# Optimization experiments

Measured on AMD Instinct MI355X. Metric: run time of the kernel, lower is better.

## Reference

```python
import jax, jax.numpy as jnp
import numpy as np

EMBED_DIM = 1024
NUM_HEADS = 16
HEAD_DIM = EMBED_DIM // NUM_HEADS
THETA = 10000.0


def setup_inputs() -> dict:
    key = jax.random.key(0)
    ks = jax.random.split(key, 5)
    B, S, E = 2, 2048, EMBED_DIM
    x = jax.random.normal(ks[0], (B, S, E), dtype=jnp.float32)
    s = 1.0 / np.sqrt(E)
    Wq = jax.random.normal(ks[1], (E, E), dtype=jnp.float32) * s
    Wk = jax.random.normal(ks[2], (E, E), dtype=jnp.float32) * s
    Wv = jax.random.normal(ks[3], (E, E), dtype=jnp.float32) * s
    Wo = jax.random.normal(ks[4], (E, E), dtype=jnp.float32) * s
    bo = jnp.zeros((E,), dtype=jnp.float32)
    return {"x": x, "Wq": Wq, "Wk": Wk, "Wv": Wv, "Wo": Wo, "bo": bo}


def _apply_rope(t, cos, sin):
    # t: (B, H, S, D); cos, sin: (S, D/2)
    t1 = t[..., 0::2]
    t2 = t[..., 1::2]
    r1 = t1 * cos - t2 * sin
    r2 = t1 * sin + t2 * cos
    # interleave back: (..., D/2, 2) -> (..., D)
    return jnp.stack([r1, r2], axis=-1).reshape(t.shape)


def reference(x, Wq, Wk, Wv, Wo, bo):
    B, S, E = x.shape
    H, D = NUM_HEADS, HEAD_DIM
    scale = D ** -0.5

    # projections (torch Linear: y = x @ W.T)
    q = (x @ Wq.T).reshape(B, S, H, D).transpose(0, 2, 1, 3)
    k = (x @ Wk.T).reshape(B, S, H, D).transpose(0, 2, 1, 3)
    v = (x @ Wv.T).reshape(B, S, H, D).transpose(0, 2, 1, 3)

    # fixed RoPE freqs (temporal, non-learned)
    freqs = 1.0 / THETA ** (jnp.arange(0, D, 2, dtype=jnp.float32) / D)  # (D/2,)
    pos = jnp.arange(S, dtype=jnp.float32)
    angles = pos[:, None] * freqs[None, :]  # (S, D/2)
    cos, sin = jnp.cos(angles), jnp.sin(angles)

    q = _apply_rope(q, cos, sin)
    k = _apply_rope(k, cos, sin)

    attn = jnp.einsum('bhqd,bhkd->bhqk', q, k) * scale
    attn = jax.nn.softmax(attn, axis=-1)
    out = jnp.einsum('bhqk,bhkd->bhqd', attn, v)
    out = out.transpose(0, 2, 1, 3).reshape(B, S, E)
    return out @ Wo.T + bo
```

## Files before the change

kernel.cpp:

```cpp
#include <hip/hip_runtime.h>


typedef __attribute__((ext_vector_type(8))) short bf16x8;
typedef __attribute__((ext_vector_type(4))) float f32x4;
typedef unsigned short u16;
typedef unsigned int u32;

#define MFMA(a, b, c) __builtin_amdgcn_mfma_f32_16x16x32_bf16((a), (b), (c), 0, 0, 0)

#define GLOAD16(g, l)                                                        \
  __builtin_amdgcn_global_load_lds((const __attribute__((address_space(1))) void*)(g), \
                                   (__attribute__((address_space(3))) void*)(l), 16, 0, 0)

__device__ __forceinline__ float bf2f(u16 u) {
  union { u32 i; float f; } v; v.i = ((u32)u) << 16; return v.f;
}
__device__ __forceinline__ u16 f2bf(float f) {
  union { float f; u32 i; } v; v.f = f;
  u32 x = v.i;
  return (u16)((x + 0x7fffu + ((x >> 16) & 1u)) >> 16);
}

__global__ __launch_bounds__(256) void prep_kernel(
    const float* __restrict__ x, const float* __restrict__ Wq, const float* __restrict__ Wk,
    const float* __restrict__ Wv, const float* __restrict__ Wo, u16* __restrict__ xb,
    u16* __restrict__ Wqb, u16* __restrict__ Wkb, u16* __restrict__ Wvb, u16* __restrict__ Wob,
    float* __restrict__ cosT, float* __restrict__ sinT) {
  int bid = blockIdx.x;
  if (bid < 4096) {
    int i = bid * 256 + threadIdx.x;
    const float* src;
    u16* dst;
    int r;
    if (i < 524288) {
      src = x; dst = xb; r = i;
    } else {
      int k = i - 524288, sel = k >> 17;
      r = k & 131071;
      src = sel == 0 ? Wq : sel == 1 ? Wk : sel == 2 ? Wv : Wo;
      dst = sel == 0 ? Wqb : sel == 1 ? Wkb : sel == 2 ? Wvb : Wob;
    }
    const float4* p = (const float4*)src + 2 * (size_t)r;
    float4 a = p[0], b = p[1];
    bf16x8 o;
    o[0] = (short)f2bf(a.x); o[1] = (short)f2bf(a.y);
    o[2] = (short)f2bf(a.z); o[3] = (short)f2bf(a.w);
    o[4] = (short)f2bf(b.x); o[5] = (short)f2bf(b.y);
    o[6] = (short)f2bf(b.z); o[7] = (short)f2bf(b.w);
    *(bf16x8*)(dst + 8 * (size_t)r) = o;
  } else {
    int i = (bid - 4096) * 256 + threadIdx.x;
    int s = i >> 5, p = i & 31;
    float freq = powf(10000.0f, -(float)(2 * p) / 64.0f);
    float ang = (float)s * freq;
    cosT[i] = cosf(ang);
    sinT[i] = sinf(ang);
  }
}

template <int MODE>
__global__ __launch_bounds__(256) void gemm_bt_kernel(
    const u16* __restrict__ A, const u16* __restrict__ B0, const u16* __restrict__ B1,
    const u16* __restrict__ B2, u16* __restrict__ Qo, u16* __restrict__ Ko,
    u16* __restrict__ VT, const float* __restrict__ cosT, const float* __restrict__ sinT,
    float* __restrict__ Cf, const float* __restrict__ bias, int Ntot) {
  const int K = 1024;
  const int tid = threadIdx.x, lane = tid & 63, wid = tid >> 6;
  const int wr = wid >> 1, wc = wid & 1;
  const int m0 = blockIdx.y * 128;
  const int nt = blockIdx.x;
  const int n0 = nt * 128;
  const u16* Bt;
  int nloc0, sel;
  if (MODE == 0) {
    sel = nt >> 3;
    Bt = sel == 0 ? B0 : (sel == 1 ? B1 : B2);
    nloc0 = n0 & 1023;
  } else {
    sel = 0;
    Bt = B0;
    nloc0 = n0;
  }

  __shared__ u16 As[128 * 64];
  __shared__ u16 Bs[128 * 64];

  f32x4 acc[4][4];
#pragma unroll
  for (int i = 0; i < 4; i++)
#pragma unroll
    for (int j = 0; j < 4; j++) acc[i][j] = f32x4{0.f, 0.f, 0.f, 0.f};

  const int strow = tid >> 3;
  const int sgcol0 = (tid & 7) * 8;

  auto stage = [&](int k0) {
#pragma unroll
    for (int p = 0; p < 4; ++p) {
      int row = p * 32 + strow;
      int gcol = sgcol0 ^ ((row & 7) << 3);
      const u16* ga = A + (size_t)(m0 + row) * K + k0 + gcol;
      const u16* gb = Bt + (size_t)(nloc0 + row) * K + k0 + gcol;
      u16* la = As + (p * 256 + wid * 64) * 8;
      u16* lb = Bs + (p * 256 + wid * 64) * 8;
      GLOAD16(ga, la);
      GLOAD16(gb, lb);
    }
  };

  for (int k0 = 0; k0 < K; k0 += 64) {
    stage(k0);
    __syncthreads();
#pragma unroll
    for (int kk = 0; kk < 2; ++kk) {
      bf16x8 af[4], bfr[4];
#pragma unroll
      for (int i = 0; i < 4; ++i) {
        int row = wr * 64 + i * 16 + (lane & 15);
        int col = (kk * 32 + (lane >> 4) * 8) ^ ((row & 7) << 3);
        af[i] = *(const bf16x8*)(As + row * 64 + col);
      }
#pragma unroll
      for (int j = 0; j < 4; ++j) {
        int row = wc * 64 + j * 16 + (lane & 15);
        int col = (kk * 32 + (lane >> 4) * 8) ^ ((row & 7) << 3);
        bfr[j] = *(const bf16x8*)(Bs + row * 64 + col);
      }
#pragma unroll
      for (int i = 0; i < 4; ++i)
#pragma unroll
        for (int j = 0; j < 4; ++j) acc[i][j] = MFMA(af[i], bfr[j], acc[i][j]);
    }
    __syncthreads();
  }

  if (MODE == 1) {
#pragma unroll
    for (int i = 0; i < 4; ++i)
#pragma unroll
      for (int j = 0; j < 4; ++j)
#pragma unroll
        for (int r = 0; r < 4; ++r) {
          int row = m0 + wr * 64 + i * 16 + (lane >> 4) * 4 + r;
          int col = n0 + wc * 64 + j * 16 + (lane & 15);
          Cf[(size_t)row * Ntot + col] = acc[i][j][r] + bias[col];
        }
    return;
  }

  const int par = lane & 1;
  if (sel < 2) {
    u16* dst = sel == 0 ? Qo : Ko;
    const float mul = sel == 0 ? 0.125f : 1.0f;
#pragma unroll
    for (int i = 0; i < 4; ++i) {
      int rowb = m0 + wr * 64 + i * 16 + (lane >> 4) * 4;
      int s = rowb & 2047, b = rowb >> 11;
#pragma unroll
      for (int j = 0; j < 4; ++j) {
        int col = nloc0 + wc * 64 + j * 16 + (lane & 15);
        int h = col >> 6, dd = col & 63, p = dd >> 1;
        size_t base = ((size_t)(b * 16 + h) * 2048 + s) * 64 + (dd & ~1);
#pragma unroll
        for (int r = 0; r < 4; ++r) {
          float v = acc[i][j][r];
          float other = __shfl_xor(v, 1, 64);
          float t1 = par ? other : v;
          float t2 = par ? v : other;
          float c = cosT[(s + r) * 32 + p];
          float sn = sinT[(s + r) * 32 + p];
          float r0 = (t1 * c - t2 * sn) * mul;
          float r1 = (t1 * sn + t2 * c) * mul;
          if (!par) {
            u32 pk = (u32)f2bf(r0) | ((u32)f2bf(r1) << 16);
            *(u32*)(dst + base + (size_t)r * 64) = pk;
          }
        }
      }
    }
  } else {
#pragma unroll
    for (int i = 0; i < 4; ++i) {
      int rowb = m0 + wr * 64 + i * 16 + (lane >> 4) * 4;
      int s = rowb & 2047, b = rowb >> 11;
#pragma unroll
      for (int j = 0; j < 4; ++j) {
        int col = nloc0 + wc * 64 + j * 16 + (lane & 15);
        int h = col >> 6, dd = col & 63;
        ushort4 pk;
        pk.x = f2bf(acc[i][j][0]);
        pk.y = f2bf(acc[i][j][1]);
        pk.z = f2bf(acc[i][j][2]);
        pk.w = f2bf(acc[i][j][3]);
        *(ushort4*)(VT + ((size_t)(b * 16 + h) * 64 + dd) * 2048 + s) = pk;
      }
    }
  }
}

__global__ __launch_bounds__(256) void attn_kernel(
    const u16* __restrict__ Q, const u16* __restrict__ Kk, const u16* __restrict__ VT,
    u16* __restrict__ O) {
  const int qt = blockIdx.x, bh = blockIdx.y;
  const int tid = threadIdx.x, lane = tid & 63, wid = tid >> 6;
  const int b = bh >> 4, h = bh & 15;

  __shared__ u16 Ks[2][64 * 64];
  __shared__ u16 Vs[2][64 * 64];
  __shared__ u16 Ps[4][16 * 64];

  const int qrow = qt * 64 + wid * 16 + (lane & 15);
  const size_t qbase = ((size_t)bh * 2048 + qrow) * 64;
  bf16x8 qf[2];
  qf[0] = *(const bf16x8*)(Q + qbase + (lane >> 4) * 8);
  qf[1] = *(const bf16x8*)(Q + qbase + 32 + (lane >> 4) * 8);

  f32x4 o[4];
#pragma unroll
  for (int j = 0; j < 4; ++j) o[j] = f32x4{0.f, 0.f, 0.f, 0.f};
  float lsum[4] = {0.f, 0.f, 0.f, 0.f};

  const u16* Kb = Kk + (size_t)bh * 2048 * 64;
  const u16* Vb = VT + (size_t)bh * 64 * 2048;

  const int strow = tid >> 3;
  const int sgc0 = (tid & 7) * 8;
  auto stage = [&](int t, int buf) {
#pragma unroll
    for (int p = 0; p < 2; ++p) {
      int row = p * 32 + strow;
      int gcol = sgc0 ^ ((row & 7) << 3);
      const u16* gk = Kb + (size_t)(t * 64 + row) * 64 + gcol;
      const u16* gv = Vb + (size_t)row * 2048 + t * 64 + gcol;
      u16* lk = Ks[buf] + (p * 256 + wid * 64) * 8;
      u16* lv = Vs[buf] + (p * 256 + wid * 64) * 8;
      GLOAD16(gk, lk);
      GLOAD16(gv, lv);
    }
  };

  stage(0, 0);
  char* Pw = (char*)&Ps[wid][0];
  for (int t = 0; t < 32; ++t) {
    const int buf = t & 1;
    __syncthreads();
    if (t + 1 < 32) stage(t + 1, buf ^ 1);

    f32x4 sc4[4];
#pragma unroll
    for (int j = 0; j < 4; ++j) sc4[j] = f32x4{0.f, 0.f, 0.f, 0.f};
#pragma unroll
    for (int kk = 0; kk < 2; ++kk) {
      bf16x8 kf[4];
#pragma unroll
      for (int j = 0; j < 4; ++j) {
        int row = j * 16 + (lane & 15);
        int col = (kk * 32 + (lane >> 4) * 8) ^ ((row & 7) << 3);
        kf[j] = *(const bf16x8*)(Ks[buf] + row * 64 + col);
      }
#pragma unroll
      for (int j = 0; j < 4; ++j) sc4[j] = MFMA(qf[kk], kf[j], sc4[j]);
    }

#pragma unroll
    for (int j = 0; j < 4; ++j)
#pragma unroll
      for (int r = 0; r < 4; ++r) {
        float pv = __expf(sc4[j][r] - 24.0f);
        union { float f; u32 i; } uu;
        uu.f = pv;
        u32 bits = uu.i;
        uu.i = bits & 0xffff0000u;
        lsum[r] += uu.f;
        int prow = (lane >> 4) * 4 + r, pcol = j * 16 + (lane & 15);
        int off = (prow * 128 + pcol * 2) ^ ((prow & 7) << 4);
        *(u16*)(Pw + off) = (u16)(bits >> 16);
      }

#pragma unroll
    for (int kk = 0; kk < 2; ++kk) {
      int prow = lane & 15;
      int poff = (prow * 128 + kk * 64 + (lane >> 4) * 16) ^ ((prow & 7) << 4);
      bf16x8 pf = *(const bf16x8*)(Pw + poff);
      bf16x8 vf[4];
#pragma unroll
      for (int j = 0; j < 4; ++j) {
        int vrow = j * 16 + (lane & 15);
        int vcol = (kk * 32 + (lane >> 4) * 8) ^ ((vrow & 7) << 3);
        vf[j] = *(const bf16x8*)(Vs[buf] + vrow * 64 + vcol);
      }
#pragma unroll
      for (int j = 0; j < 4; ++j) o[j] = MFMA(pf, vf[j], o[j]);
    }
  }

#pragma unroll
  for (int r = 0; r < 4; ++r) {
#pragma unroll
    for (int d = 1; d < 16; d <<= 1) lsum[r] += __shfl_xor(lsum[r], d, 64);
  }

#pragma unroll
  for (int j = 0; j < 4; ++j)
#pragma unroll
    for (int r = 0; r < 4; ++r) {
      int srow = qt * 64 + wid * 16 + (lane >> 4) * 4 + r;
      int col = h * 64 + j * 16 + (lane & 15);
      float val = o[j][r] * __frcp_rn(lsum[r]);
      O[(size_t)(b * 2048 + srow) * 1024 + col] = f2bf(val);
    }
}

extern "C" void kernel_launch(void* const* d_in, const int* in_sizes, int n_in,
                              void* d_out, int out_size, void* d_ws, size_t ws_size,
                              hipStream_t stream) {
  const float* x = (const float*)d_in[0];
  const float* Wq = (const float*)d_in[1];
  const float* Wk = (const float*)d_in[2];
  const float* Wv = (const float*)d_in[3];
  const float* Wo = (const float*)d_in[4];
  const float* bo = (const float*)d_in[5];

  char* ws = (char*)d_ws;
  size_t off = 0;
  auto carve = [&](size_t bytes) {
    void* pp = ws + off;
    off += (bytes + 255) & ~(size_t)255;
    return pp;
  };
  u16* xb = (u16*)carve(4194304ull * 2);
  u16* Wqb = (u16*)carve(1048576ull * 2);
  u16* Wkb = (u16*)carve(1048576ull * 2);
  u16* Wvb = (u16*)carve(1048576ull * 2);
  u16* Wob = (u16*)carve(1048576ull * 2);
  float* cosT = (float*)carve(65536ull * 4);
  float* sinT = (float*)carve(65536ull * 4);
  u16* q_r = (u16*)carve(4194304ull * 2);
  u16* k_r = (u16*)carve(4194304ull * 2);
  u16* vT = (u16*)carve(4194304ull * 2);
  u16* attn_out = (u16*)carve(4194304ull * 2);

  prep_kernel<<<4352, 256, 0, stream>>>(x, Wq, Wk, Wv, Wo, xb, Wqb, Wkb, Wvb, Wob, cosT, sinT);
  gemm_bt_kernel<0><<<dim3(24, 32), 256, 0, stream>>>(xb, Wqb, Wkb, Wvb, q_r, k_r, vT, cosT,
                                                      sinT, nullptr, nullptr, 3072);
  attn_kernel<<<dim3(32, 32), 256, 0, stream>>>(q_r, k_r, vT, attn_out);
  gemm_bt_kernel<1><<<dim3(8, 32), 256, 0, stream>>>(attn_out, Wob, nullptr, nullptr, nullptr,
                                                     nullptr, nullptr, nullptr, nullptr,
                                                     (float*)d_out, bo, 1024);
}
```

Measured before the change: 231.7 us.

## Double query rows per attention wave and permute Wq/Wk rows to drop RoPE shuffles

The attention kernel now gives each wave 32 query rows (two 16-row groups) instead of 16, so each K/V tile loaded into LDS and fragments read from it are reused across twice as many MFMAs, with half as many blocks. Separately, the prep kernel permutes Wq/Wk rows so that even/odd RoPE pairs land in separate MFMA column tiles held by the same lane. This removes the cross-lane shuffle and the half-idle stores in the QKV epilogue, and cos/sin tables are transposed so each lane loads them as float4. The cost is higher register pressure and fewer attention blocks (512) to fill the GPU.

New measurement: 211.9 us. 1.09x faster.

```diff
diff --git a/kernel.cpp b/kernel.cpp
--- a/kernel.cpp
+++ b/kernel.cpp
@@ -31,11 +31,12 @@
     int i = bid * 256 + threadIdx.x;
     const float* src;
     u16* dst;
-    int r;
+    int r, sel;
     if (i < 524288) {
-      src = x; dst = xb; r = i;
+      src = x; dst = xb; r = i; sel = -1;
     } else {
-      int k = i - 524288, sel = k >> 17;
+      int k = i - 524288;
+      sel = k >> 17;
       r = k & 131071;
       src = sel == 0 ? Wq : sel == 1 ? Wk : sel == 2 ? Wv : Wo;
       dst = sel == 0 ? Wqb : sel == 1 ? Wkb : sel == 2 ? Wvb : Wob;
@@ -47,10 +48,18 @@
     o[2] = (short)f2bf(a.z); o[3] = (short)f2bf(a.w);
     o[4] = (short)f2bf(b.x); o[5] = (short)f2bf(b.y);
     o[6] = (short)f2bf(b.z); o[7] = (short)f2bf(b.w);
-    *(bf16x8*)(dst + 8 * (size_t)r) = o;
+    int outr = r;
+    if (sel == 0 || sel == 1) {
+      int row = r >> 7, kc = r & 127;
+      int h = row >> 6, dd = row & 63;
+      int u = dd & 1, pp = dd >> 1, half = pp >> 4, c = pp & 15;
+      int g = 16 * (2 * half + u) + c;
+      outr = (h * 64 + g) * 128 + kc;
+    }
+    *(bf16x8*)(dst + 8 * (size_t)outr) = o;
   } else {
     int i = (bid - 4096) * 256 + threadIdx.x;
-    int s = i >> 5, p = i & 31;
+    int p = i >> 11, s = i & 2047;
     float freq = powf(10000.0f, -(float)(2 * p) / 64.0f);
     float ang = (float)s * freq;
     cosT[i] = cosf(ang);
@@ -148,7 +157,8 @@
     return;
   }
 
-  const int par = lane & 1;
+  const int c = lane & 15;
+  const int hh = (nloc0 + wc * 64) >> 6;
   if (sel < 2) {
     u16* dst = sel == 0 ? Qo : Ko;
     const float mul = sel == 0 ? 0.125f : 1.0f;
@@ -156,25 +166,20 @@
     for (int i = 0; i < 4; ++i) {
       int rowb = m0 + wr * 64 + i * 16 + (lane >> 4) * 4;
       int s = rowb & 2047, b = rowb >> 11;
-#pragma unroll
-      for (int j = 0; j < 4; ++j) {
-        int col = nloc0 + wc * 64 + j * 16 + (lane & 15);
-        int h = col >> 6, dd = col & 63, p = dd >> 1;
-        size_t base = ((size_t)(b * 16 + h) * 2048 + s) * 64 + (dd & ~1);
+      size_t obase = ((size_t)(b * 16 + hh) * 2048 + s) * 64;
+#pragma unroll
+      for (int half = 0; half < 2; ++half) {
+        int p = half * 16 + c;
+        float4 c4 = *(const float4*)(cosT + p * 2048 + s);
+        float4 s4 = *(const float4*)(sinT + p * 2048 + s);
 #pragma unroll
         for (int r = 0; r < 4; ++r) {
-          float v = acc[i][j][r];
-          float other = __shfl_xor(v, 1, 64);
-          float t1 = par ? other : v;
-          float t2 = par ? v : other;
-          float c = cosT[(s + r) * 32 + p];
-          float sn = sinT[(s + r) * 32 + p];
-          float r0 = (t1 * c - t2 * sn) * mul;
-          float r1 = (t1 * sn + t2 * c) * mul;
-          if (!par) {
-            u32 pk = (u32)f2bf(r0) | ((u32)f2bf(r1) << 16);
-            *(u32*)(dst + base + (size_t)r * 64) = pk;
-          }
+          float t1 = acc[i][2 * half][r], t2 = acc[i][2 * half + 1][r];
+          float cc = (&c4.x)[r], ss = (&s4.x)[r];
+          float r0 = (t1 * cc - t2 * ss) * mul;
+          float r1 = (t1 * ss + t2 * cc) * mul;
+          u32 pk = (u32)f2bf(r0) | ((u32)f2bf(r1) << 16);
+          *(u32*)(dst + obase + (size_t)r * 64 + 2 * p) = pk;
         }
       }
     }
@@ -185,14 +190,13 @@
       int s = rowb & 2047, b = rowb >> 11;
 #pragma unroll
       for (int j = 0; j < 4; ++j) {
-        int col = nloc0 + wc * 64 + j * 16 + (lane & 15);
-        int h = col >> 6, dd = col & 63;
+        int dd = j * 16 + c;
         ushort4 pk;
         pk.x = f2bf(acc[i][j][0]);
         pk.y = f2bf(acc[i][j][1]);
         pk.z = f2bf(acc[i][j][2]);
         pk.w = f2bf(acc[i][j][3]);
-        *(ushort4*)(VT + ((size_t)(b * 16 + h) * 64 + dd) * 2048 + s) = pk;
+        *(ushort4*)(VT + ((size_t)(b * 16 + hh) * 64 + dd) * 2048 + s) = pk;
       }
     }
   }
@@ -207,18 +211,23 @@
 
   __shared__ u16 Ks[2][64 * 64];
   __shared__ u16 Vs[2][64 * 64];
-  __shared__ u16 Ps[4][16 * 64];
-
-  const int qrow = qt * 64 + wid * 16 + (lane & 15);
-  const size_t qbase = ((size_t)bh * 2048 + qrow) * 64;
-  bf16x8 qf[2];
-  qf[0] = *(const bf16x8*)(Q + qbase + (lane >> 4) * 8);
-  qf[1] = *(const bf16x8*)(Q + qbase + 32 + (lane >> 4) * 8);
-
-  f32x4 o[4];
-#pragma unroll
-  for (int j = 0; j < 4; ++j) o[j] = f32x4{0.f, 0.f, 0.f, 0.f};
-  float lsum[4] = {0.f, 0.f, 0.f, 0.f};
+  __shared__ u16 Ps[4][32 * 64];
+
+  const int qrow0 = qt * 128 + wid * 32;
+  bf16x8 qf[2][2];
+#pragma unroll
+  for (int g = 0; g < 2; ++g) {
+    const size_t qbase = ((size_t)bh * 2048 + qrow0 + g * 16 + (lane & 15)) * 64;
+    qf[g][0] = *(const bf16x8*)(Q + qbase + (lane >> 4) * 8);
+    qf[g][1] = *(const bf16x8*)(Q + qbase + 32 + (lane >> 4) * 8);
+  }
+
+  f32x4 o[2][4];
+#pragma unroll
+  for (int g = 0; g < 2; ++g)
+#pragma unroll
+    for (int j = 0; j < 4; ++j) o[g][j] = f32x4{0.f, 0.f, 0.f, 0.f};
+  float lsum[2][4] = {{0.f, 0.f, 0.f, 0.f}, {0.f, 0.f, 0.f, 0.f}};
 
   const u16* Kb = Kk + (size_t)bh * 2048 * 64;
   const u16* Vb = VT + (size_t)bh * 64 * 2048;
@@ -246,69 +255,84 @@
     __syncthreads();
     if (t + 1 < 32) stage(t + 1, buf ^ 1);
 
-    f32x4 sc4[4];
-#pragma unroll
-    for (int j = 0; j < 4; ++j) sc4[j] = f32x4{0.f, 0.f, 0.f, 0.f};
-#pragma unroll
-    for (int kk = 0; kk < 2; ++kk) {
-      bf16x8 kf[4];
+    bf16x8 kf[2][4];
+#pragma unroll
+    for (int kk = 0; kk < 2; ++kk)
 #pragma unroll
       for (int j = 0; j < 4; ++j) {
         int row = j * 16 + (lane & 15);
         int col = (kk * 32 + (lane >> 4) * 8) ^ ((row & 7) << 3);
-        kf[j] = *(const bf16x8*)(Ks[buf] + row * 64 + col);
-      }
-#pragma unroll
-      for (int j = 0; j < 4; ++j) sc4[j] = MFMA(qf[kk], kf[j], sc4[j]);
-    }
-
-#pragma unroll
-    for (int j = 0; j < 4; ++j)
-#pragma unroll
-      for (int r = 0; r < 4; ++r) {
-        float pv = __expf(sc4[j][r] - 24.0f);
-        union { float f; u32 i; } uu;
-        uu.f = pv;
-        u32 bits = uu.i;
-        uu.i = bits & 0xffff0000u;
-        lsum[r] += uu.f;
-        int prow = (lane >> 4) * 4 + r, pcol = j * 16 + (lane & 15);
-        int off = (prow * 128 + pcol * 2) ^ ((prow & 7) << 4);
-        *(u16*)(Pw + off) = (u16)(bits >> 16);
-      }
-
-#pragma unroll
-    for (int kk = 0; kk < 2; ++kk) {
-      int prow = lane & 15;
-      int poff = (prow * 128 + kk * 64 + (lane >> 4) * 16) ^ ((prow & 7) << 4);
-      bf16x8 pf = *(const bf16x8*)(Pw + poff);
-      bf16x8 vf[4];
+        kf[kk][j] = *(const bf16x8*)(Ks[buf] + row * 64 + col);
+      }
+
+    f32x4 sc4[2][4];
+#pragma unroll
+    for (int g = 0; g < 2; ++g)
+#pragma unroll
+      for (int j = 0; j < 4; ++j) sc4[g][j] = f32x4{0.f, 0.f, 0.f, 0.f};
+#pragma unroll
+    for (int kk = 0; kk < 2; ++kk)
+#pragma unroll
+      for (int g = 0; g < 2; ++g)
+#pragma unroll
+        for (int j = 0; j < 4; ++j) sc4[g][j] = MFMA(qf[g][kk], kf[kk][j], sc4[g][j]);
+
+#pragma unroll
+    for (int g = 0; g < 2; ++g)
+#pragma unroll
+      for (int j = 0; j < 4; ++j)
+#pragma unroll
+        for (int r = 0; r < 4; ++r) {
+          float pv = __expf(sc4[g][j][r] - 24.0f);
+          union { float f; u32 i; } uu;
+          uu.f = pv;
+          u32 bits = uu.i;
+          uu.i = bits & 0xffff0000u;
+          lsum[g][r] += uu.f;
+          int prow = g * 16 + (lane >> 4) * 4 + r;
+          int off = (prow * 128 + (j * 16 + (lane & 15)) * 2) ^ ((prow & 7) << 4);
+          *(u16*)(Pw + off) = (u16)(bits >> 16);
+        }
+
+    bf16x8 vf[2][4];
+#pragma unroll
+    for (int kk = 0; kk < 2; ++kk)
 #pragma unroll
       for (int j = 0; j < 4; ++j) {
         int vrow = j * 16 + (lane & 15);
         int vcol = (kk * 32 + (lane >> 4) * 8) ^ ((vrow & 7) << 3);
-        vf[j] = *(const bf16x8*)(Vs[buf] + vrow * 64 + vcol);
-      }
-#pragma unroll
-      for (int j = 0; j < 4; ++j) o[j] = MFMA(pf, vf[j], o[j]);
-    }
-  }
-
-#pragma unroll
-  for (int r = 0; r < 4; ++r) {
-#pragma unroll
-    for (int d = 1; d < 16; d <<= 1) lsum[r] += __shfl_xor(lsum[r], d, 64);
-  }
-
-#pragma unroll
-  for (int j = 0; j < 4; ++j)
+        vf[kk][j] = *(const bf16x8*)(Vs[buf] + vrow * 64 + vcol);
+      }
+
+#pragma unroll
+    for (int g = 0; g < 2; ++g)
+#pragma unroll
+      for (int kk = 0; kk < 2; ++kk) {
+        int prow = g * 16 + (lane & 15);
+        int poff = (prow * 128 + kk * 64 + (lane >> 4) * 16) ^ ((prow & 7) << 4);
+        bf16x8 pf = *(const bf16x8*)(Pw + poff);
+#pragma unroll
+        for (int j = 0; j < 4; ++j) o[g][j] = MFMA(pf, vf[kk][j], o[g][j]);
+      }
+  }
+
+#pragma unroll
+  for (int g = 0; g < 2; ++g) {
 #pragma unroll
     for (int r = 0; r < 4; ++r) {
-      int srow = qt * 64 + wid * 16 + (lane >> 4) * 4 + r;
-      int col = h * 64 + j * 16 + (lane & 15);
-      float val = o[j][r] * __frcp_rn(lsum[r]);
-      O[(size_t)(b * 2048 + srow) * 1024 + col] = f2bf(val);
-    }
+#pragma unroll
+      for (int d = 1; d < 16; d <<= 1) lsum[g][r] += __shfl_xor(lsum[g][r], d, 64);
+    }
+#pragma unroll
+    for (int j = 0; j < 4; ++j)
+#pragma unroll
+      for (int r = 0; r < 4; ++r) {
+        int srow = qrow0 + g * 16 + (lane >> 4) * 4 + r;
+        int col = h * 64 + j * 16 + (lane & 15);
+        float val = o[g][j][r] * __frcp_rn(lsum[g][r]);
+        O[(size_t)(b * 2048 + srow) * 1024 + col] = f2bf(val);
+      }
+  }
 }
 
 extern "C" void kernel_launch(void* const* d_in, const int* in_sizes, int n_in,
@@ -343,7 +367,7 @@
   prep_kernel<<<4352, 256, 0, stream>>>(x, Wq, Wk, Wv, Wo, xb, Wqb, Wkb, Wvb, Wob, cosT, sinT);
   gemm_bt_kernel<0><<<dim3(24, 32), 256, 0, stream>>>(xb, Wqb, Wkb, Wvb, q_r, k_r, vT, cosT,
                                                       sinT, nullptr, nullptr, 3072);
-  attn_kernel<<<dim3(32, 32), 256, 0, stream>>>(q_r, k_r, vT, attn_out);
+  attn_kernel<<<dim3(16, 32), 256, 0, stream>>>(q_r, k_r, vT, attn_out);
   gemm_bt_kernel<1><<<dim3(8, 32), 256, 0, stream>>>(attn_out, Wob, nullptr, nullptr, nullptr,
                                                      nullptr, nullptr, nullptr, nullptr,
                                                      (float*)d_out, bo, 1024);
```
